# Kernel optimization log

Measured on AMD Instinct MI355X. Metric: run time of the kernel, lower is better.

The kernel has to match this reference:

```python
import jax, jax.numpy as jnp
import numpy as np

P = 7  # corr_size
P2 = P * P
NEG_SLOPE = 0.01  # default LeakyReLU


def _correlate(f1, f2):
    """spatial_correlation_sample with kernel_size=1, stride=1, padding=0,
    dilation_patch=1: out[b,pi,pj,y,x] = sum_c f1[b,c,y,x] * f2[b,c,y+pi-r,x+pj-r]
    (zero padded), returned flattened to [b, P*P, h, w]."""
    r = P // 2
    b, c, h, w = f1.shape
    f2p = jnp.pad(f2, ((0, 0), (0, 0), (r, r), (r, r)))
    outs = []
    for pi in range(P):
        for pj in range(P):
            sh = jax.lax.slice(f2p, (0, 0, pi, pj), (b, c, pi + h, pj + w))
            outs.append(jnp.sum(f1 * sh, axis=1))  # [b,h,w]
    return jnp.stack(outs, axis=1)  # [b, P*P, h, w]


def _conv3x3(x, w, b):
    y = jax.lax.conv_general_dilated(
        x, w, window_strides=(1, 1), padding=((1, 1), (1, 1)),
        dimension_numbers=('NCHW', 'OIHW', 'NCHW'))
    return y + b[None, :, None, None]


def _up_nearest(x, s):
    return jnp.repeat(jnp.repeat(x, s, axis=2), s, axis=3)


def _level(feat1, feat2, h_pre, c_pre, w, b, scale):
    # feat1 = current frame (x), feat2 = previous frame (x_pre)
    u1 = _up_nearest(feat1, scale)
    u2 = _up_nearest(feat2, scale)
    corr = _correlate(u1, u2)                        # [B, P*P, H*s, W*s]
    corr = jnp.where(corr >= 0, corr, NEG_SLOPE * corr)  # leaky relu
    dw = corr[:, :, ::scale, ::scale]                # nearest downsample back
    lstm_in = jnp.concatenate([dw, h_pre], axis=1)   # [B, 2*P*P, H, W]
    conv = _conv3x3(lstm_in, w, b)                   # [B, 4*P*P, H, W]
    cc_i, cc_f, cc_o, cc_g = jnp.split(conv, 4, axis=1)
    i = jax.nn.sigmoid(cc_i)
    f = jax.nn.sigmoid(cc_f)
    o = jax.nn.sigmoid(cc_o)
    g = jnp.tanh(cc_g)
    c_next = f * c_pre + i * g
    h_next = o * jnp.tanh(c_next)
    return h_next, c_next


def setup_inputs() -> dict:
    key = jax.random.key(0)
    ks = jax.random.split(key, 10)
    x0 = jax.random.normal(ks[0], (2, 512, 64, 64), jnp.float32) * 0.1
    x1 = jax.random.normal(ks[1], (2, 1024, 32, 32), jnp.float32) * 0.1
    xp0 = jax.random.normal(ks[2], (2, 512, 64, 64), jnp.float32) * 0.1
    xp1 = jax.random.normal(ks[3], (2, 1024, 32, 32), jnp.float32) * 0.1
    h0 = jax.random.normal(ks[4], (2, P2, 64, 64), jnp.float32) * 0.1
    c0 = jax.random.normal(ks[5], (2, P2, 64, 64), jnp.float32) * 0.1
    h1 = jax.random.normal(ks[6], (2, P2, 32, 32), jnp.float32) * 0.1
    c1 = jax.random.normal(ks[7], (2, P2, 32, 32), jnp.float32) * 0.1
    w0 = jax.random.normal(ks[8], (4 * P2, 2 * P2, 3, 3), jnp.float32) * 0.02
    w1 = jax.random.normal(ks[9], (4 * P2, 2 * P2, 3, 3), jnp.float32) * 0.02
    # init_weights sets the forget-gate bias slice to 1
    b0 = jnp.zeros((4 * P2,), jnp.float32).at[P2:2 * P2].set(1.0)
    b1 = jnp.zeros((4 * P2,), jnp.float32).at[P2:2 * P2].set(1.0)
    return {"x0": x0, "x1": x1, "xp0": xp0, "xp1": xp1,
            "h0": h0, "c0": c0, "h1": h1, "c1": c1,
            "w0": w0, "b0": b0, "w1": w1, "b1": b1}


def reference(x0, x1, xp0, xp1, h0, c0, h1, c1, w0, b0, w1, b1):
    # level i: upsample scale = upsample_param * 2**i = 2 * 2**i
    h0n, c0n = _level(x0, xp0, h0, c0, w0, b0, scale=2)
    h1n, c1n = _level(x1, xp1, h1, c1, w1, b1, scale=4)
    return (h0n, c0n, h1n, c1n)
```

## Files before the change

kernel.cpp:

```cpp
#include <hip/hip_runtime.h>

#define DEVFN __device__ __forceinline__

typedef __attribute__((ext_vector_type(8))) __bf16 bf16x8;
typedef __attribute__((ext_vector_type(16))) float f32x16;
typedef unsigned short ushort;

DEVFN float sigmoidf_(float x) { return 1.f / (1.f + __expf(-x)); }

DEVFN ushort f2bf(float f) {
    unsigned u = __float_as_uint(f);
    unsigned r = (u + 0x7FFF + ((u >> 16) & 1)) >> 16;
    return (ushort)r;
}

template<int C, int CC, int H, int W, int NOFF, int OFS>
__global__ __launch_bounds__(256, 1) void corr_kernel(const float* __restrict__ f1,
                                                      const float* __restrict__ f2,
                                                      float* __restrict__ slices) {
    constexpr int HW = H * W;
    constexpr int WIN = NOFF + 3;
    const int t     = threadIdx.x;
    const int px    = blockIdx.x * 1024 + t * 4;
    const int b     = blockIdx.y;
    const int chunk = blockIdx.z;
    const int y  = px / W;
    const int x0 = px - y * W;

    const float* f1p    = f1 + ((size_t)b * C + chunk * CC) * HW + px;
    const float* f2b    = f2 + ((size_t)b * C + chunk * CC) * HW;
    const float* f2lo   = f2;
    const float* f2hi   = f2 + (size_t)2 * C * HW - 2;

    int   yc[NOFF];
    float rm[NOFF];
#pragma unroll
    for (int d = 0; d < NOFF; ++d) {
        int yy = y + d - OFS;
        rm[d] = (yy >= 0 && yy < H) ? 1.f : 0.f;
        yc[d] = yy < 0 ? 0 : (yy >= H ? H - 1 : yy);
    }

    float acc[NOFF][NOFF][4];
#pragma unroll
    for (int i = 0; i < NOFF; ++i)
#pragma unroll
        for (int j = 0; j < NOFF; ++j)
#pragma unroll
            for (int p = 0; p < 4; ++p) acc[i][j][p] = 0.f;

#pragma unroll 2
    for (int c = 0; c < CC; ++c) {
        float f1a[4];
        *reinterpret_cast<float4*>(f1a) = *reinterpret_cast<const float4*>(f1p + (size_t)c * HW);
        float w[NOFF][WIN];
#pragma unroll
        for (int d = 0; d < NOFF; ++d) {
            const float* r = f2b + (size_t)c * HW + yc[d] * W + x0;
            if constexpr (OFS == 2) {
                const float* plo = (r - 2 < f2lo) ? f2lo : (r - 2);
                const float* phi = (r + 4 > f2hi) ? f2hi : (r + 4);
                float2 lo = *reinterpret_cast<const float2*>(plo);
                float4 md = *reinterpret_cast<const float4*>(r);
                float  hv = *phi;
                w[d][0] = lo.x; w[d][1] = lo.y;
                w[d][2] = md.x; w[d][3] = md.y; w[d][4] = md.z; w[d][5] = md.w;
                w[d][6] = hv;
            } else {
                const float* plo = (r - 1 < f2lo) ? f2lo : (r - 1);
                float  lv = *plo;
                float4 md = *reinterpret_cast<const float4*>(r);
                w[d][0] = lv;
                w[d][1] = md.x; w[d][2] = md.y; w[d][3] = md.z; w[d][4] = md.w;
            }
        }
#pragma unroll
        for (int d = 0; d < NOFF; ++d)
#pragma unroll
            for (int dx = 0; dx < NOFF; ++dx)
#pragma unroll
                for (int p = 0; p < 4; ++p)
                    acc[d][dx][p] = fmaf(f1a[p], w[d][p + dx], acc[d][dx][p]);
    }

    float* ao = slices + ((size_t)(chunk * 2 + b) * NOFF * NOFF) * HW + px;
#pragma unroll
    for (int dyi = 0; dyi < NOFF; ++dyi)
#pragma unroll
        for (int dxi = 0; dxi < NOFF; ++dxi) {
            float v[4];
#pragma unroll
            for (int p = 0; p < 4; ++p) {
                int col = x0 + p + dxi - OFS;
                float m = (col >= 0 && col < W) ? rm[dyi] : 0.f;
                v[p] = acc[dyi][dxi][p] * m;
            }
            *reinterpret_cast<float4*>(ao + (size_t)(dyi * NOFF + dxi) * HW) =
                make_float4(v[0], v[1], v[2], v[3]);
        }
}

template<int S, int STRIDE>
__global__ void reduce_kernel(const float* __restrict__ in, float* __restrict__ out) {
    const int i = (blockIdx.x * 256 + threadIdx.x) * 4;
    if (i >= STRIDE) return;
    float sx = 0.f, sy = 0.f, sz = 0.f, sw = 0.f;
#pragma unroll 8
    for (int k = 0; k < S; ++k) {
        float4 v = *reinterpret_cast<const float4*>(in + (size_t)k * STRIDE + i);
        sx += v.x; sy += v.y; sz += v.z; sw += v.w;
    }
    *reinterpret_cast<float4*>(out + i) = make_float4(sx, sy, sz, sw);
}

template<int H, int W, int SCALE, int SHIFT, int NOFF, int OFS>
__global__ void xbuild_kernel(const float* __restrict__ base, const float* __restrict__ h_pre,
                              ushort* __restrict__ Xin) {
    const int HW = H * W;
    int i = blockIdx.x * 256 + threadIdx.x;
    if (i >= 2 * HW * 16) return;
    int g  = i & 15;
    int px = (i >> 4) % HW;
    int b  = (i >> 4) / HW;
    int y = px / W, x = px - y * W;
    ushort out8[8];
#pragma unroll
    for (int j = 0; j < 8; ++j) {
        int ic = g * 8 + j;
        float v = 0.f;
        if (ic < 49) {
            int pi = ic / 7, pj = ic - pi * 7;
            int dy = pi - 3, dx = pj - 3;
            int uy = SCALE * y + dy, ux = SCALE * x + dx;
            if (uy >= 0 && uy < SCALE * H && ux >= 0 && ux < SCALE * W) {
                int idy = (dy >> SHIFT) + OFS;
                int idx = (dx >> SHIFT) + OFS;
                float cv = base[((size_t)b * NOFF * NOFF + idy * NOFF + idx) * HW + px];
                v = cv >= 0.f ? cv : 0.01f * cv;
            }
        } else if (ic < 98) {
            v = h_pre[((size_t)b * 49 + (ic - 49)) * HW + px];
        }
        out8[j] = f2bf(v);
    }
    size_t off = (((size_t)b * 8 + (g >> 1)) * HW + px) * 16 + (g & 1) * 8;
    *reinterpret_cast<uint4*>(Xin + off) = *reinterpret_cast<uint4*>(out8);
}

__global__ void wprep_kernel(const float* __restrict__ w0, const float* __restrict__ w1,
                             ushort* __restrict__ Wmf0, ushort* __restrict__ Wmf1) {
    const float* w = blockIdx.y ? w1 : w0;
    ushort* Wmf    = blockIdx.y ? Wmf1 : Wmf0;
    int i = blockIdx.x * 256 + threadIdx.x;
    const int n = 9 * 16 * 256 * 8;
    if (i >= n) return;
    int iEl = i & 7;
    int oc  = (i >> 3) & 255;
    int icg = (i >> 11) & 15;
    int tap = i >> 15;
    int ic  = icg * 8 + iEl;
    float v = (oc < 196 && ic < 98) ? w[((size_t)oc * 98 + ic) * 9 + tap] : 0.f;
    Wmf[i] = f2bf(v);
}

template<int H, int W, int SPLIT, int ICPS, int NKC>
__global__ __launch_bounds__(256, 2) void convmf_kernel(const ushort* __restrict__ Xin,
                                                        const ushort* __restrict__ Wmf,
                                                        float* __restrict__ Y) {
    const int HW = H * W;
    const int tilesx = W / 16;
    const int by0 = (blockIdx.x / tilesx) * 8;
    const int bx0 = (blockIdx.x % tilesx) * 16;
    const int ocb = blockIdx.y * 64;
    const int b   = blockIdx.z & 1;
    const int s   = blockIdx.z >> 1;
    const int t   = threadIdx.x;
    const int wv  = t >> 6;
    const int l   = t & 63;
    const int n    = l & 31;
    const int hi   = l >> 5;
    const int wrow = 2 * wv + (n >> 4);
    const int wcol = n & 15;

    f32x16 acc0 = {};
    f32x16 acc1 = {};

#pragma unroll
    for (int kc = 0; kc < NKC; ++kc) {
        const int icg8  = (s * ICPS + kc * 16) / 8 + hi;
        const int icg16 = (s * ICPS) / 16 + kc;
        const ushort* wp = Wmf + ((size_t)icg8 * 256 + ocb + n) * 8;
        const ushort* xb = Xin + ((size_t)b * 8 + icg16) * HW * 16 + hi * 8;
#pragma unroll
        for (int j = 0; j < 9; ++j) {
            const int ky = j / 3, kx = j - ky * 3;
            bf16x8 a0 = *reinterpret_cast<const bf16x8*>(wp + (size_t)j * 16 * 256 * 8);
            bf16x8 a1 = *reinterpret_cast<const bf16x8*>(wp + (size_t)j * 16 * 256 * 8 + 32 * 8);
            const int gy = by0 + wrow + ky - 1;
            const int gx = bx0 + wcol + kx - 1;
            bf16x8 bfr = {};
            if (gy >= 0 && gy < H && gx >= 0 && gx < W)
                bfr = *reinterpret_cast<const bf16x8*>(xb + (size_t)(gy * W + gx) * 16);
            acc0 = __builtin_amdgcn_mfma_f32_32x32x16_bf16(a0, bfr, acc0, 0, 0, 0);
            acc1 = __builtin_amdgcn_mfma_f32_32x32x16_bf16(a1, bfr, acc1, 0, 0, 0);
        }
    }

    float* Yo = Y + ((size_t)(s * 2 + b) * 196) * HW;
    const int po = (by0 + wrow) * W + bx0 + wcol;
#pragma unroll
    for (int r = 0; r < 16; ++r) {
        int m = (r & 3) + 8 * (r >> 2) + 4 * hi;
        int oc0 = ocb + m;
        if (oc0 < 196) Yo[(size_t)oc0 * HW + po] = acc0[r];
        int oc1 = ocb + 32 + m;
        if (oc1 < 196) Yo[(size_t)oc1 * HW + po] = acc1[r];
    }
}

template<int S, int HW>
__global__ void lstm_kernel(const float* __restrict__ Y, const float* __restrict__ bias,
                            const float* __restrict__ c_pre,
                            float* __restrict__ h_out, float* __restrict__ c_out) {
    int i = blockIdx.x * 256 + threadIdx.x;
    const int n = 2 * 49 * HW;
    if (i >= n) return;
    int b   = i / (49 * HW);
    int rem = i - b * (49 * HW);
    int k   = rem / HW;
    float g4[4];
#pragma unroll
    for (int gi = 0; gi < 4; ++gi) {
        float v = bias[gi * 49 + k];
#pragma unroll
        for (int ss = 0; ss < S; ++ss)
            v += Y[((size_t)((ss * 2 + b) * 196) + gi * 49) * HW + rem];
        g4[gi] = v;
    }
    float iv = sigmoidf_(g4[0]);
    float fv = sigmoidf_(g4[1]);
    float ov = sigmoidf_(g4[2]);
    float gv = tanhf(g4[3]);
    float cp = c_pre[i];
    float cn = fv * cp + iv * gv;
    h_out[i] = ov * tanhf(cn);
    c_out[i] = cn;
}

extern "C" void kernel_launch(void* const* d_in, const int* in_sizes, int n_in,
                              void* d_out, int out_size, void* d_ws, size_t ws_size,
                              hipStream_t stream) {
    (void)in_sizes; (void)n_in; (void)out_size; (void)ws_size;
    const float* x0  = (const float*)d_in[0];
    const float* x1  = (const float*)d_in[1];
    const float* xp0 = (const float*)d_in[2];
    const float* xp1 = (const float*)d_in[3];
    const float* h0  = (const float*)d_in[4];
    const float* c0  = (const float*)d_in[5];
    const float* h1  = (const float*)d_in[6];
    const float* c1  = (const float*)d_in[7];
    const float* w0  = (const float*)d_in[8];
    const float* b0  = (const float*)d_in[9];
    const float* w1  = (const float*)d_in[10];
    const float* b1  = (const float*)d_in[11];
    float* out = (float*)d_out;

    float* ws = (float*)d_ws;
    float*  Wmf0f = ws;
    float*  Wmf1f = Wmf0f + 147456;
    float*  Xin0f = Wmf1f + 147456;
    float*  Xin1f = Xin0f + 524288;
    float*  base0 = Xin1f + 131072;
    float*  base1 = base0 + 131072;
    float*  Y0    = base1 + 8192;
    float*  Y1    = Y0 + 3211264;
    float*  slc0  = Y0;
    float*  slc1  = Y0 + 4194304;
    ushort* Wmf0 = (ushort*)Wmf0f;
    ushort* Wmf1 = (ushort*)Wmf1f;
    ushort* Xin0 = (ushort*)Xin0f;
    ushort* Xin1 = (ushort*)Xin1f;

    corr_kernel<512, 16, 64, 64, 4, 2><<<dim3(4, 2, 32), 256, 0, stream>>>(x0, xp0, slc0);
    corr_kernel<1024, 16, 32, 32, 2, 1><<<dim3(1, 2, 64), 256, 0, stream>>>(x1, xp1, slc1);

    reduce_kernel<32, 131072><<<128, 256, 0, stream>>>(slc0, base0);
    reduce_kernel<64, 8192><<<8, 256, 0, stream>>>(slc1, base1);

    wprep_kernel<<<dim3(1152, 2), 256, 0, stream>>>(w0, w1, Wmf0, Wmf1);

    xbuild_kernel<64, 64, 2, 1, 4, 2><<<512, 256, 0, stream>>>(base0, h0, Xin0);
    xbuild_kernel<32, 32, 4, 2, 2, 1><<<128, 256, 0, stream>>>(base1, h1, Xin1);

    convmf_kernel<64, 64, 2, 64, 4><<<dim3(32, 4, 4), 256, 0, stream>>>(Xin0, Wmf0, Y0);
    convmf_kernel<32, 32, 4, 32, 2><<<dim3(8, 4, 8), 256, 0, stream>>>(Xin1, Wmf1, Y1);

    lstm_kernel<2, 4096><<<1568, 256, 0, stream>>>(Y0, b0, c0, out + 0,      out + 401408);
    lstm_kernel<4, 1024><<<392,  256, 0, stream>>>(Y1, b1, c1, out + 802816, out + 903168);
}
```

Baseline: 189.4 us.

## Double split-K across correlation and conv, widen conv tile, restructure corr loads

The correlation kernel now processes half as many channels per block (8 instead of 16) across twice as many blocks, and loads each f2 row window just before using it instead of preloading all rows. This cuts register pressure enough to allow two blocks per CU. The MFMA conv kernel now computes a 32-wide pixel tile per block with four accumulators, and is split over twice as many input-channel slices. The reduce and LSTM kernels are resized to sum the extra partials, and the workspace is relaid so slices and conv outputs no longer alias. The cost is more partial-sum traffic through global memory in exchange for more parallel blocks and occupancy.

```diff
diff --git a/kernel.cpp b/kernel.cpp
--- a/kernel.cpp
+++ b/kernel.cpp
@@ -15,7 +15,7 @@
 }
 
 template<int C, int CC, int H, int W, int NOFF, int OFS>
-__global__ __launch_bounds__(256, 1) void corr_kernel(const float* __restrict__ f1,
+__global__ __launch_bounds__(256, 2) void corr_kernel(const float* __restrict__ f1,
                                                       const float* __restrict__ f2,
                                                       float* __restrict__ slices) {
     constexpr int HW = H * W;
@@ -53,34 +53,32 @@
     for (int c = 0; c < CC; ++c) {
         float f1a[4];
         *reinterpret_cast<float4*>(f1a) = *reinterpret_cast<const float4*>(f1p + (size_t)c * HW);
-        float w[NOFF][WIN];
 #pragma unroll
         for (int d = 0; d < NOFF; ++d) {
             const float* r = f2b + (size_t)c * HW + yc[d] * W + x0;
+            float w[WIN];
             if constexpr (OFS == 2) {
                 const float* plo = (r - 2 < f2lo) ? f2lo : (r - 2);
                 const float* phi = (r + 4 > f2hi) ? f2hi : (r + 4);
                 float2 lo = *reinterpret_cast<const float2*>(plo);
                 float4 md = *reinterpret_cast<const float4*>(r);
                 float  hv = *phi;
-                w[d][0] = lo.x; w[d][1] = lo.y;
-                w[d][2] = md.x; w[d][3] = md.y; w[d][4] = md.z; w[d][5] = md.w;
-                w[d][6] = hv;
+                w[0] = lo.x; w[1] = lo.y;
+                w[2] = md.x; w[3] = md.y; w[4] = md.z; w[5] = md.w;
+                w[6] = hv;
             } else {
                 const float* plo = (r - 1 < f2lo) ? f2lo : (r - 1);
                 float  lv = *plo;
                 float4 md = *reinterpret_cast<const float4*>(r);
-                w[d][0] = lv;
-                w[d][1] = md.x; w[d][2] = md.y; w[d][3] = md.z; w[d][4] = md.w;
+                w[0] = lv;
+                w[1] = md.x; w[2] = md.y; w[3] = md.z; w[4] = md.w;
             }
-        }
-#pragma unroll
-        for (int d = 0; d < NOFF; ++d)
 #pragma unroll
             for (int dx = 0; dx < NOFF; ++dx)
 #pragma unroll
                 for (int p = 0; p < 4; ++p)
-                    acc[d][dx][p] = fmaf(f1a[p], w[d][p + dx], acc[d][dx][p]);
+                    acc[d][dx][p] = fmaf(f1a[p], w[p + dx], acc[d][dx][p]);
+        }
     }
 
     float* ao = slices + ((size_t)(chunk * 2 + b) * NOFF * NOFF) * HW + px;
@@ -168,9 +166,9 @@
                                                         const ushort* __restrict__ Wmf,
                                                         float* __restrict__ Y) {
     const int HW = H * W;
-    const int tilesx = W / 16;
+    const int tilesx = W / 32;
     const int by0 = (blockIdx.x / tilesx) * 8;
-    const int bx0 = (blockIdx.x % tilesx) * 16;
+    const int bx0 = (blockIdx.x % tilesx) * 32;
     const int ocb = blockIdx.y * 64;
     const int b   = blockIdx.z & 1;
     const int s   = blockIdx.z >> 1;
@@ -182,27 +180,30 @@
     const int wrow = 2 * wv + (n >> 4);
     const int wcol = n & 15;
 
-    f32x16 acc0 = {};
-    f32x16 acc1 = {};
+    f32x16 acc00 = {}, acc10 = {}, acc01 = {}, acc11 = {};
 
 #pragma unroll
     for (int kc = 0; kc < NKC; ++kc) {
         const int icg8  = (s * ICPS + kc * 16) / 8 + hi;
         const int icg16 = (s * ICPS) / 16 + kc;
         const ushort* wp = Wmf + ((size_t)icg8 * 256 + ocb + n) * 8;
-        const ushort* xb = Xin + ((size_t)b * 8 + icg16) * HW * 16 + hi * 8;
+        const ushort* xb = Xin + (((size_t)b * 8 + icg16) * HW) * 16 + hi * 8;
 #pragma unroll
         for (int j = 0; j < 9; ++j) {
             const int ky = j / 3, kx = j - ky * 3;
             bf16x8 a0 = *reinterpret_cast<const bf16x8*>(wp + (size_t)j * 16 * 256 * 8);
             bf16x8 a1 = *reinterpret_cast<const bf16x8*>(wp + (size_t)j * 16 * 256 * 8 + 32 * 8);
-            const int gy = by0 + wrow + ky - 1;
-            const int gx = bx0 + wcol + kx - 1;
-            bf16x8 bfr = {};
-            if (gy >= 0 && gy < H && gx >= 0 && gx < W)
-                bfr = *reinterpret_cast<const bf16x8*>(xb + (size_t)(gy * W + gx) * 16);
-            acc0 = __builtin_amdgcn_mfma_f32_32x32x16_bf16(a0, bfr, acc0, 0, 0, 0);
-            acc1 = __builtin_amdgcn_mfma_f32_32x32x16_bf16(a1, bfr, acc1, 0, 0, 0);
+            const int gy  = by0 + wrow + ky - 1;
+            const int gx0 = bx0 + wcol + kx - 1;
+            const int gx1 = gx0 + 16;
+            const bool yok = (gy >= 0) && (gy < H);
+            bf16x8 bf0 = {}, bf1 = {};
+            if (yok && gx0 >= 0 && gx0 < W) bf0 = *reinterpret_cast<const bf16x8*>(xb + (size_t)(gy * W + gx0) * 16);
+            if (yok && gx1 < W)             bf1 = *reinterpret_cast<const bf16x8*>(xb + (size_t)(gy * W + gx1) * 16);
+            acc00 = __builtin_amdgcn_mfma_f32_32x32x16_bf16(a0, bf0, acc00, 0, 0, 0);
+            acc10 = __builtin_amdgcn_mfma_f32_32x32x16_bf16(a1, bf0, acc10, 0, 0, 0);
+            acc01 = __builtin_amdgcn_mfma_f32_32x32x16_bf16(a0, bf1, acc01, 0, 0, 0);
+            acc11 = __builtin_amdgcn_mfma_f32_32x32x16_bf16(a1, bf1, acc11, 0, 0, 0);
         }
     }
 
@@ -212,9 +213,15 @@
     for (int r = 0; r < 16; ++r) {
         int m = (r & 3) + 8 * (r >> 2) + 4 * hi;
         int oc0 = ocb + m;
-        if (oc0 < 196) Yo[(size_t)oc0 * HW + po] = acc0[r];
         int oc1 = ocb + 32 + m;
-        if (oc1 < 196) Yo[(size_t)oc1 * HW + po] = acc1[r];
+        if (oc0 < 196) {
+            Yo[(size_t)oc0 * HW + po]      = acc00[r];
+            Yo[(size_t)oc0 * HW + po + 16] = acc01[r];
+        }
+        if (oc1 < 196) {
+            Yo[(size_t)oc1 * HW + po]      = acc10[r];
+            Yo[(size_t)oc1 * HW + po + 16] = acc11[r];
+        }
     }
 }
 
@@ -272,29 +279,29 @@
     float*  Xin1f = Xin0f + 524288;
     float*  base0 = Xin1f + 131072;
     float*  base1 = base0 + 131072;
-    float*  Y0    = base1 + 8192;
-    float*  Y1    = Y0 + 3211264;
-    float*  slc0  = Y0;
-    float*  slc1  = Y0 + 4194304;
+    float*  slc0  = base1 + 8192;
+    float*  slc1  = slc0 + 8388608;
+    float*  Y0    = slc1 + 1048576;
+    float*  Y1    = Y0 + 6422528;
     ushort* Wmf0 = (ushort*)Wmf0f;
     ushort* Wmf1 = (ushort*)Wmf1f;
     ushort* Xin0 = (ushort*)Xin0f;
     ushort* Xin1 = (ushort*)Xin1f;
 
-    corr_kernel<512, 16, 64, 64, 4, 2><<<dim3(4, 2, 32), 256, 0, stream>>>(x0, xp0, slc0);
-    corr_kernel<1024, 16, 32, 32, 2, 1><<<dim3(1, 2, 64), 256, 0, stream>>>(x1, xp1, slc1);
-
-    reduce_kernel<32, 131072><<<128, 256, 0, stream>>>(slc0, base0);
-    reduce_kernel<64, 8192><<<8, 256, 0, stream>>>(slc1, base1);
+    corr_kernel<512, 8, 64, 64, 4, 2><<<dim3(4, 2, 64), 256, 0, stream>>>(x0, xp0, slc0);
+    corr_kernel<1024, 8, 32, 32, 2, 1><<<dim3(1, 2, 128), 256, 0, stream>>>(x1, xp1, slc1);
+
+    reduce_kernel<64, 131072><<<128, 256, 0, stream>>>(slc0, base0);
+    reduce_kernel<128, 8192><<<8, 256, 0, stream>>>(slc1, base1);
 
     wprep_kernel<<<dim3(1152, 2), 256, 0, stream>>>(w0, w1, Wmf0, Wmf1);
 
     xbuild_kernel<64, 64, 2, 1, 4, 2><<<512, 256, 0, stream>>>(base0, h0, Xin0);
     xbuild_kernel<32, 32, 4, 2, 2, 1><<<128, 256, 0, stream>>>(base1, h1, Xin1);
 
-    convmf_kernel<64, 64, 2, 64, 4><<<dim3(32, 4, 4), 256, 0, stream>>>(Xin0, Wmf0, Y0);
-    convmf_kernel<32, 32, 4, 32, 2><<<dim3(8, 4, 8), 256, 0, stream>>>(Xin1, Wmf1, Y1);
-
-    lstm_kernel<2, 4096><<<1568, 256, 0, stream>>>(Y0, b0, c0, out + 0,      out + 401408);
-    lstm_kernel<4, 1024><<<392,  256, 0, stream>>>(Y1, b1, c1, out + 802816, out + 903168);
-}
+    convmf_kernel<64, 64, 4, 32, 2><<<dim3(16, 4, 8), 256, 0, stream>>>(Xin0, Wmf0, Y0);
+    convmf_kernel<32, 32, 8, 16, 1><<<dim3(4, 4, 16), 256, 0, stream>>>(Xin1, Wmf1, Y1);
+
+    lstm_kernel<4, 4096><<<1568, 256, 0, stream>>>(Y0, b0, c0, out + 0,      out + 401408);
+    lstm_kernel<8, 1024><<<392,  256, 0, stream>>>(Y1, b1, c1, out + 802816, out + 903168);
+}
```

Result: no change. 186.7 us (-1.4%).
